# Performance work log

Measured on AMD Instinct MI355X. Metric: run time of the kernel, lower is better.

Reference implementation:

```python
import jax, jax.numpy as jnp
import numpy as np

T = 2048
C = 2048
N_HEAD = 16
HEAD_DIM = C // N_HEAD


def setup_inputs() -> dict:
    key = jax.random.key(0)
    k1, k2, k3 = jax.random.split(key, 3)
    x = jax.random.normal(k1, (T, C), dtype=jnp.float32)
    # eqx.nn.Linear weight convention: (out_features, in_features)
    W_attn = jax.random.normal(k2, (3 * C, C), dtype=jnp.float32) * (1.0 / np.sqrt(C))
    W_proj = jax.random.normal(k3, (C, C), dtype=jnp.float32) * (1.0 / np.sqrt(C))
    return {"x": x, "W_attn": W_attn, "W_proj": W_proj}


def reference(x, W_attn, W_proj):
    # qkv projection: (T, 3C)
    qkv = x @ W_attn.T
    q, k, v = jnp.split(qkv, 3, axis=-1)
    # reshape to (H, T, d)
    q = q.reshape(T, N_HEAD, HEAD_DIM).transpose(1, 0, 2)
    k = k.reshape(T, N_HEAD, HEAD_DIM).transpose(1, 0, 2)
    v = v.reshape(T, N_HEAD, HEAD_DIM).transpose(1, 0, 2)
    # scaled causal attention: (H, T, T)
    att = jnp.einsum('htd,hsd->hts', q, k)
    causal_mask = jnp.triu(jnp.ones((T, T), dtype=bool), k=1)  # mask future keys
    att = jnp.where(causal_mask, -jnp.inf, att)
    att = jax.nn.softmax(att / jnp.sqrt(jnp.float32(HEAD_DIM)), axis=-1)
    # attention output: (H, T, d) -> (T, C)
    out = jnp.einsum('hts,hsd->htd', att, v)
    out = out.transpose(1, 0, 2).reshape(T, C)
    return out @ W_proj.T
```

## Files before the change

kernel.cpp:

```cpp
#include <hip/hip_runtime.h>
#include <cstdint>

using bx8 = __attribute__((ext_vector_type(8))) __bf16;
using us8 = __attribute__((ext_vector_type(8))) unsigned short;
using us4 = __attribute__((ext_vector_type(4))) unsigned short;
using fl8 = __attribute__((ext_vector_type(8))) float;
using fx4 = __attribute__((ext_vector_type(4))) float;

static __device__ inline unsigned short f2bf(float f) {
  unsigned u = __builtin_bit_cast(unsigned, f);
  unsigned r = 0x7FFFu + ((u >> 16) & 1u);
  return (unsigned short)((u + r) >> 16);
}
static __device__ inline float bf2f(unsigned short s) {
  return __builtin_bit_cast(float, (unsigned)s << 16);
}

static __device__ inline fx4 mfma16(bx8 a, bx8 b, fx4 c) {
  return __builtin_amdgcn_mfma_f32_16x16x32_bf16(a, b, c, 0, 0, 0);
}

static __device__ inline void gload16(const void* g, void* lds) {
  __builtin_amdgcn_global_load_lds(
      (const __attribute__((address_space(1))) void*)g,
      (__attribute__((address_space(3))) void*)lds,
      16, 0, 0);
}
#define VMCNT(n) asm volatile("s_waitcnt vmcnt(" #n ")" ::: "memory")
static __device__ inline void wave_barrier() {
  __builtin_amdgcn_sched_barrier(0);
  __builtin_amdgcn_s_barrier();
  __builtin_amdgcn_sched_barrier(0);
}

#define DPP_ROR(x, k) __builtin_bit_cast(float, __builtin_amdgcn_update_dpp( \
    __builtin_bit_cast(int, x), __builtin_bit_cast(int, x), 0x120 | (k), 0xF, 0xF, false))

static __device__ inline float rowmax16(float v) {
  v = fmaxf(v, DPP_ROR(v, 1));
  v = fmaxf(v, DPP_ROR(v, 2));
  v = fmaxf(v, DPP_ROR(v, 4));
  v = fmaxf(v, DPP_ROR(v, 8));
  return v;
}
static __device__ inline float rowsum16(float v) {
  v += DPP_ROR(v, 1);
  v += DPP_ROR(v, 2);
  v += DPP_ROR(v, 4);
  v += DPP_ROR(v, 8);
  return v;
}

__global__ __launch_bounds__(256) void f2b_kernel(const float* __restrict__ in,
                                                  unsigned short* __restrict__ out,
                                                  int n) {
  int i = (blockIdx.x * 256 + threadIdx.x) * 4;
  if (i >= n) return;
  float4 v = *reinterpret_cast<const float4*>(in + i);
  ushort4 o;
  o.x = f2bf(v.x); o.y = f2bf(v.y); o.z = f2bf(v.z); o.w = f2bf(v.w);
  *reinterpret_cast<ushort4*>(out + i) = o;
}

__global__ __launch_bounds__(512, 2) void gemm256(const unsigned short* __restrict__ A,
                                                  const unsigned short* __restrict__ B,
                                                  unsigned short* __restrict__ C,
                                                  int M, int N, int K) {
  __shared__ unsigned short lds[4][2][256 * 32];

  const int tid = threadIdx.x;
  const int w = tid >> 6, l = tid & 63;
  const int l16 = l & 15, lg = l >> 4;
  const int wr = w >> 2, wc = w & 3;
  const long mb = (long)blockIdx.y * 256, nb = (long)blockIdx.x * 256;

  const int lr = l >> 2;
  const int sw = (((l & 3) ^ (lr & 3)) * 8);
  const unsigned short* Ag = A + (mb + w * 32 + lr) * (long)K + sw;
  const unsigned short* Bg = B + (nb + w * 32 + lr) * (long)K + sw;

  const int rdcol = ((lg ^ (l16 & 3)) * 16);

  const fx4 fz = {0.f, 0.f, 0.f, 0.f};
  fx4 acc[8][4];
#pragma unroll
  for (int i = 0; i < 8; ++i)
#pragma unroll
    for (int j = 0; j < 4; ++j) acc[i][j] = fz;

  const int nt = K >> 5;

  auto stage = [&](int tp) {
    const int db = tp & 3;
    const unsigned short* as = Ag + tp * 32;
    const unsigned short* bs = Bg + tp * 32;
    char* al = (char*)&lds[db][0][0] + w * 32 * 64;
    char* bl = (char*)&lds[db][1][0] + w * 32 * 64;
    gload16(as, al);
    gload16(as + 16 * (long)K, al + 1024);
    gload16(bs, bl);
    gload16(bs + 16 * (long)K, bl + 1024);
  };

  auto compute = [&](int bt) {
    const char* Ab = (const char*)&lds[bt][0][0] + (wr * 128 + l16) * 64 + rdcol;
    const char* Bb = (const char*)&lds[bt][1][0] + (wc * 64 + l16) * 64 + rdcol;
    bx8 bf[4];
#pragma unroll
    for (int nf = 0; nf < 4; ++nf)
      bf[nf] = *reinterpret_cast<const bx8*>(Bb + nf * 1024);
    __builtin_amdgcn_s_setprio(1);
#pragma unroll
    for (int mf = 0; mf < 8; ++mf) {
      bx8 av = *reinterpret_cast<const bx8*>(Ab + mf * 1024);
#pragma unroll
      for (int nf = 0; nf < 4; ++nf)
        acc[mf][nf] = mfma16(av, bf[nf], acc[mf][nf]);
    }
    __builtin_amdgcn_s_setprio(0);
  };

  stage(0); stage(1); stage(2);
  VMCNT(8);
  wave_barrier();

  int t = 0;
  for (; t < nt - 3; ++t) {
    stage(t + 3);
    compute(t & 3);
    VMCNT(8);
    wave_barrier();
  }
  compute(t & 3); VMCNT(4); wave_barrier(); ++t;
  compute(t & 3); VMCNT(0); wave_barrier(); ++t;
  compute(t & 3);

#pragma unroll
  for (int mf = 0; mf < 8; ++mf)
#pragma unroll
    for (int nf = 0; nf < 4; ++nf)
#pragma unroll
      for (int r = 0; r < 4; ++r) {
        const long row = mb + wr * 128 + mf * 16 + lg * 4 + r;
        const long col = nb + wc * 64 + nf * 16 + l16;
        C[row * N + col] = f2bf(acc[mf][nf][r]);
      }
}

template <typename T> struct RegOf { using type = us8; };
template <> struct RegOf<float>  { using type = fl8; };

template <typename T>
static __device__ inline typename RegOf<T>::type load8(const T* p) {
  return *reinterpret_cast<const typename RegOf<T>::type*>(p);
}
static __device__ inline us8 toBf(us8 v) { return v; }
static __device__ inline us8 toBf(fl8 f) {
  us8 o;
#pragma unroll
  for (int j = 0; j < 8; ++j) {
    __bf16 b = (__bf16)f[j];
    o[j] = __builtin_bit_cast(unsigned short, b);
  }
  return o;
}

template <typename TA, typename TB, bool F32OUT>
__global__ __launch_bounds__(256) void gemm_bt(const TA* __restrict__ A,
                                               const TB* __restrict__ B,
                                               void* __restrict__ Cp,
                                               int M, int N, int K) {
  __shared__ alignas(16) unsigned short As[128 * 64];
  __shared__ alignas(16) unsigned short Bs[128 * 64];
  const int tid = threadIdx.x;
  const int w = tid >> 6, l = tid & 63;
  const int l16 = l & 15, lg = l >> 4;
  const int wr = w >> 1, wc = w & 1;
  const long mb = (long)blockIdx.y * 128, nb = (long)blockIdx.x * 128;

  const fx4 fz = {0.f, 0.f, 0.f, 0.f};
  fx4 acc[4][4];
#pragma unroll
  for (int i = 0; i < 4; ++i)
#pragma unroll
    for (int j = 0; j < 4; ++j) acc[i][j] = fz;

  const int sr  = tid >> 3;
  const int sc8 = (tid & 7) * 8;
  const int wbc = sc8 * 2;

  typename RegOf<TA>::type rA[4];
  typename RegOf<TB>::type rB[4];

#pragma unroll
  for (int p = 0; p < 4; ++p) {
    const int row = p * 32 + sr;
    rA[p] = load8(A + (mb + row) * (long)K + sc8);
    rB[p] = load8(B + (nb + row) * (long)K + sc8);
  }

  for (int k0 = 0; k0 < K; k0 += 64) {
    __syncthreads();
#pragma unroll
    for (int p = 0; p < 4; ++p) {
      const int row = p * 32 + sr;
      const int eo = row * 64 + ((wbc ^ ((row & 7) << 4)) >> 1);
      *reinterpret_cast<us8*>(&As[eo]) = toBf(rA[p]);
      *reinterpret_cast<us8*>(&Bs[eo]) = toBf(rB[p]);
    }
    if (k0 + 64 < K) {
#pragma unroll
      for (int p = 0; p < 4; ++p) {
        const int row = p * 32 + sr;
        rA[p] = load8(A + (mb + row) * (long)K + k0 + 64 + sc8);
        rB[p] = load8(B + (nb + row) * (long)K + k0 + 64 + sc8);
      }
    }
    __syncthreads();
#pragma unroll
    for (int kk = 0; kk < 2; ++kk) {
      bx8 a[4], b[4];
#pragma unroll
      for (int mf = 0; mf < 4; ++mf) {
        const int ra = wr * 64 + mf * 16 + l16;
        const int bc = kk * 64 + lg * 16;
        a[mf] = *reinterpret_cast<const bx8*>(&As[ra * 64 + ((bc ^ ((ra & 7) << 4)) >> 1)]);
      }
#pragma unroll
      for (int nf = 0; nf < 4; ++nf) {
        const int rb_ = wc * 64 + nf * 16 + l16;
        const int bc = kk * 64 + lg * 16;
        b[nf] = *reinterpret_cast<const bx8*>(&Bs[rb_ * 64 + ((bc ^ ((rb_ & 7) << 4)) >> 1)]);
      }
#pragma unroll
      for (int mf = 0; mf < 4; ++mf)
#pragma unroll
        for (int nf = 0; nf < 4; ++nf)
          acc[mf][nf] = mfma16(a[mf], b[nf], acc[mf][nf]);
    }
  }

#pragma unroll
  for (int mf = 0; mf < 4; ++mf)
#pragma unroll
    for (int nf = 0; nf < 4; ++nf)
#pragma unroll
      for (int r = 0; r < 4; ++r) {
        const long row = mb + wr * 64 + mf * 16 + lg * 4 + r;
        const long col = nb + wc * 64 + nf * 16 + l16;
        if (F32OUT)
          ((float*)Cp)[row * N + col] = acc[mf][nf][r];
        else
          ((unsigned short*)Cp)[row * N + col] = f2bf(acc[mf][nf][r]);
      }
}

__global__ __launch_bounds__(256) void fa_kernel(const unsigned short* __restrict__ qkv,
                                                 unsigned short* __restrict__ Obuf,
                                                 float* __restrict__ ML) {
  __shared__ alignas(16) char smem[40960];

  const int id = blockIdx.x;
  const int h = id & 15, i = id >> 4;
  int qt, ck;
  if (i < 32)      { qt = 31 - (i >> 2); ck = i & 3; }
  else if (i < 56) { const int j = i - 32; qt = 23 - j / 3; ck = j % 3; }
  else if (i < 72) { const int j = i - 56; qt = 15 - (j >> 1); ck = j & 1; }
  else             { qt = 7 - (i - 72); ck = 0; }
  const int t0 = ck * 8;
  const int t1 = min(t0 + 8, qt + 1);
  const int qb = qt * 64;

  const int tid = threadIdx.x;
  const int w = tid >> 6, l = tid & 63;
  const int l16 = l & 15, lg = l >> 4;
  const fx4 fz = {0.f, 0.f, 0.f, 0.f};

  const int kr = tid >> 4, ksl = tid & 15;
  const int kg = tid & 15, db = tid >> 4;
  const int kc8 = ksl * 8;

  bx8 qf[4];
  {
    const long qrow = qb + w * 16 + l16;
    const unsigned short* qp = qkv + qrow * 6144L + h * 128 + lg * 8;
#pragma unroll
    for (int kc = 0; kc < 4; ++kc)
      qf[kc] = *reinterpret_cast<const bx8*>(qp + kc * 32);
  }

  fx4 o_acc[8];
#pragma unroll
  for (int i2 = 0; i2 < 8; ++i2) o_acc[i2] = fz;
  float m_r[4] = {-3e38f, -3e38f, -3e38f, -3e38f};
  float l_r[4] = {0.f, 0.f, 0.f, 0.f};

  us8 rK[4], rV[4];
  {
    const long kvb = (long)t0 * 64;
#pragma unroll
    for (int p = 0; p < 4; ++p)
      rK[p] = *reinterpret_cast<const us8*>(qkv + (kvb + p * 16 + kr) * 6144L + 2048 + h * 128 + kc8);
#pragma unroll
    for (int p = 0; p < 4; ++p)
      rV[p] = *reinterpret_cast<const us8*>(qkv + (kvb + kg * 4 + p) * 6144L + 4096 + h * 128 + db * 8);
  }

  const float sc2 = 0.1275173831f;
  char* const psb = smem + 32768 + w * 2048;

  for (int t = t0; t < t1; ++t) {
    __syncthreads();

#pragma unroll
    for (int p = 0; p < 4; ++p)
      *reinterpret_cast<us8*>(smem + (p * 16 + kr) * 256 + ((ksl ^ kr) << 4)) = rK[p];
#pragma unroll
    for (int j = 0; j < 8; ++j) {
      us4 vw = {rV[0][j], rV[1][j], rV[2][j], rV[3][j]};
      *reinterpret_cast<us4*>(smem + 16384 + (db * 8 + j) * 128 +
                              (((kg >> 1) ^ j) << 4) + ((kg & 1) << 3)) = vw;
    }

    if (t + 1 < t1) {
      const long kvb = (long)(t + 1) * 64;
#pragma unroll
      for (int p = 0; p < 4; ++p)
        rK[p] = *reinterpret_cast<const us8*>(qkv + (kvb + p * 16 + kr) * 6144L + 2048 + h * 128 + kc8);
#pragma unroll
      for (int p = 0; p < 4; ++p)
        rV[p] = *reinterpret_cast<const us8*>(qkv + (kvb + kg * 4 + p) * 6144L + 4096 + h * 128 + db * 8);
    }
    __syncthreads();

    fx4 s[4];
#pragma unroll
    for (int nf = 0; nf < 4; ++nf) s[nf] = fz;
#pragma unroll
    for (int kc = 0; kc < 4; ++kc) {
#pragma unroll
      for (int nf = 0; nf < 4; ++nf) {
        const int rl = nf * 16 + l16;
        bx8 kb = *reinterpret_cast<const bx8*>(smem + rl * 256 + (((kc * 4 + lg) ^ l16) << 4));
        s[nf] = mfma16(qf[kc], kb, s[nf]);
      }
    }

    if (t == qt) {
#pragma unroll
      for (int nf = 0; nf < 4; ++nf) {
        const int kv_abs = t * 64 + nf * 16 + l16;
#pragma unroll
        for (int r = 0; r < 4; ++r) {
          const int q_abs = qb + w * 16 + lg * 4 + r;
          if (kv_abs > q_abs) s[nf][r] = -3e38f;
        }
      }
    }

    float rm_[4];
    bool st = true;
#pragma unroll
    for (int r = 0; r < 4; ++r) {
      float rm = fmaxf(fmaxf(s[0][r], s[1][r]), fmaxf(s[2][r], s[3][r]));
      rm_[r] = rowmax16(rm);
      st = st && (rm_[r] - m_r[r] <= 62.7f);
    }
    float pv[4][4];
    if (__all(st ? 1 : 0)) {
#pragma unroll
      for (int r = 0; r < 4; ++r) {
        float rs = 0.f;
#pragma unroll
        for (int nf = 0; nf < 4; ++nf) {
          const float p = exp2f((s[nf][r] - m_r[r]) * sc2);
          pv[nf][r] = p;
          rs += p;
        }
        l_r[r] += rowsum16(rs);
      }
    } else {
#pragma unroll
      for (int r = 0; r < 4; ++r) {
        const float mn = fmaxf(m_r[r], rm_[r]);
        const float fac = exp2f((m_r[r] - mn) * sc2);
        m_r[r] = mn;
        float rs = 0.f;
#pragma unroll
        for (int nf = 0; nf < 4; ++nf) {
          const float p = exp2f((s[nf][r] - mn) * sc2);
          pv[nf][r] = p;
          rs += p;
        }
        l_r[r] = l_r[r] * fac + rowsum16(rs);
#pragma unroll
        for (int nf = 0; nf < 8; ++nf) o_acc[nf][r] *= fac;
      }
    }

#pragma unroll
    for (int nf = 0; nf < 4; ++nf)
#pragma unroll
      for (int r = 0; r < 4; ++r) {
        const int ro = lg * 4 + r;
        *reinterpret_cast<unsigned short*>(
            psb + ro * 128 + (((nf * 2 + (l16 >> 3)) ^ (ro & 7)) << 4) + ((l16 & 7) << 1)) =
            __builtin_bit_cast(unsigned short, (__bf16)pv[nf][r]);
      }

    bx8 pa[2];
#pragma unroll
    for (int kc = 0; kc < 2; ++kc)
      pa[kc] = *reinterpret_cast<const bx8*>(psb + l16 * 128 + (((kc * 4 + lg) ^ (l16 & 7)) << 4));

#pragma unroll
    for (int nf = 0; nf < 8; ++nf) {
#pragma unroll
      for (int kc = 0; kc < 2; ++kc) {
        bx8 vb = *reinterpret_cast<const bx8*>(smem + 16384 + (nf * 16 + l16) * 128 +
                                               (((kc * 4 + lg) ^ (l16 & 7)) << 4));
        o_acc[nf] = mfma16(pa[kc], vb, o_acc[nf]);
      }
    }
  }

  unsigned short* ob = Obuf + (long)id * 8192;
#pragma unroll
  for (int nf = 0; nf < 8; ++nf)
#pragma unroll
    for (int r = 0; r < 4; ++r) {
      const int row = w * 16 + lg * 4 + r;
      ob[row * 128 + nf * 16 + l16] = f2bf(o_acc[nf][r]);
    }
  if (l16 == 0) {
#pragma unroll
    for (int r = 0; r < 4; ++r) {
      const int row = w * 16 + lg * 4 + r;
      ML[((long)id * 64 + row) * 2 + 0] = m_r[r];
      ML[((long)id * 64 + row) * 2 + 1] = l_r[r];
    }
  }
}

__global__ __launch_bounds__(256) void fa_combine(const unsigned short* __restrict__ Obuf,
                                                  const float* __restrict__ ML,
                                                  unsigned short* __restrict__ out) {
  const int p = blockIdx.x;
  const int qt = p >> 4, h = p & 15;
  const int nc = (qt + 8) >> 3;
  const int tid = threadIdx.x;
  const int row = tid >> 2;
  const int c0 = (tid & 3) * 32;
  const float sc2 = 0.1275173831f;

  int ids[4];
#pragma unroll
  for (int k = 0; k < 4; ++k) {
    int ib;
    if (qt >= 24)      ib = (31 - qt) * 4 + k;
    else if (qt >= 16) ib = 32 + (23 - qt) * 3 + k;
    else if (qt >= 8)  ib = 56 + (15 - qt) * 2 + k;
    else               ib = 72 + (7 - qt);
    ids[k] = ib * 16 + h;
  }

  float mk[4], lk[4];
  float m = -3e38f;
#pragma unroll
  for (int k = 0; k < 4; ++k)
    if (k < nc) {
      mk[k] = ML[((long)ids[k] * 64 + row) * 2 + 0];
      lk[k] = ML[((long)ids[k] * 64 + row) * 2 + 1];
      m = fmaxf(m, mk[k]);
    }
  float fk[4], denom = 0.f;
#pragma unroll
  for (int k = 0; k < 4; ++k)
    if (k < nc) {
      fk[k] = exp2f((mk[k] - m) * sc2);
      denom += lk[k] * fk[k];
    }
  const float inv = 1.0f / denom;

  float acc[32];
#pragma unroll
  for (int j = 0; j < 32; ++j) acc[j] = 0.f;
#pragma unroll
  for (int k = 0; k < 4; ++k)
    if (k < nc) {
      const unsigned short* ob = Obuf + (long)ids[k] * 8192 + row * 128 + c0;
      const float f = fk[k];
#pragma unroll
      for (int jj = 0; jj < 4; ++jj) {
        us8 a = *reinterpret_cast<const us8*>(ob + jj * 8);
#pragma unroll
        for (int j2 = 0; j2 < 8; ++j2) acc[jj * 8 + j2] += bf2f(a[j2]) * f;
      }
    }

  unsigned short* dst = out + (long)(qt * 64 + row) * 2048 + h * 128 + c0;
#pragma unroll
  for (int jj = 0; jj < 4; ++jj) {
    ushort4 o0, o1;
    o0.x = f2bf(acc[jj * 8 + 0] * inv);
    o0.y = f2bf(acc[jj * 8 + 1] * inv);
    o0.z = f2bf(acc[jj * 8 + 2] * inv);
    o0.w = f2bf(acc[jj * 8 + 3] * inv);
    o1.x = f2bf(acc[jj * 8 + 4] * inv);
    o1.y = f2bf(acc[jj * 8 + 5] * inv);
    o1.z = f2bf(acc[jj * 8 + 6] * inv);
    o1.w = f2bf(acc[jj * 8 + 7] * inv);
    *reinterpret_cast<ushort4*>(dst + jj * 8) = o0;
    *reinterpret_cast<ushort4*>(dst + jj * 8 + 4) = o1;
  }
}

extern "C" void kernel_launch(void* const* d_in, const int* in_sizes, int n_in,
                              void* d_out, int out_size, void* d_ws, size_t ws_size,
                              hipStream_t stream) {
  const float* x  = (const float*)d_in[0];
  const float* Wa = (const float*)d_in[1];
  const float* Wp = (const float*)d_in[2];
  float* out = (float*)d_out;
  char* ws = (char*)d_ws;

  unsigned short* wab   = (unsigned short*)(ws);
  unsigned short* qkvb  = (unsigned short*)(ws + (24ull << 20));
  unsigned short* xb    = (unsigned short*)(ws + (48ull << 20));
  unsigned short* Obuf  = (unsigned short*)(ws);
  float*          ML    = (float*)(ws + (20ull << 20));
  unsigned short* attnb = (unsigned short*)(ws + (48ull << 20));

  f2b_kernel<<<4096, 256, 0, stream>>>(x, xb, 2048 * 2048);
  f2b_kernel<<<12288, 256, 0, stream>>>(Wa, wab, 6144 * 2048);

  gemm256<<<dim3(24, 8), 512, 0, stream>>>(xb, wab, qkvb, 2048, 6144, 2048);

  fa_kernel<<<1280, 256, 0, stream>>>(qkvb, Obuf, ML);

  fa_combine<<<512, 256, 0, stream>>>(Obuf, ML, attnb);

  gemm_bt<unsigned short, float, true><<<dim3(16, 16), 256, 0, stream>>>(attnb, Wp, (void*)out, 2048, 2048, 2048);
}
```

Before: 180.7 us.

## Double flash-attention query tile to 128 rows per block for K/V reuse

Each attention block now processes 128 query rows instead of 64, with every wave handling two 16-row query fragments that share the same K and V fragments loaded from LDS. The split-K scheduling table, Obuf/ML layout and combine kernel indexing are rewritten for the new tile size, and the grid is halved. This halves K/V global and LDS traffic per query row and amortizes the synchronisation, at the cost of double the accumulator registers (lower occupancy), wasted work on the diagonal tile pairs, and fewer blocks to fill the GPU.

After: 204.0 us. 1.13x slower.

```diff
diff --git a/kernel.cpp b/kernel.cpp
--- a/kernel.cpp
+++ b/kernel.cpp
@@ -258,18 +258,19 @@
 __global__ __launch_bounds__(256) void fa_kernel(const unsigned short* __restrict__ qkv,
                                                  unsigned short* __restrict__ Obuf,
                                                  float* __restrict__ ML) {
-  __shared__ alignas(16) char smem[40960];
+  __shared__ alignas(16) char smem[49152];
 
   const int id = blockIdx.x;
   const int h = id & 15, i = id >> 4;
-  int qt, ck;
-  if (i < 32)      { qt = 31 - (i >> 2); ck = i & 3; }
-  else if (i < 56) { const int j = i - 32; qt = 23 - j / 3; ck = j % 3; }
-  else if (i < 72) { const int j = i - 56; qt = 15 - (j >> 1); ck = j & 1; }
-  else             { qt = 7 - (i - 72); ck = 0; }
+  int tau, ck;
+  if (i < 16)      { tau = 15 - (i >> 2); ck = i & 3; }
+  else if (i < 28) { const int j = i - 16; tau = 11 - j / 3; ck = j % 3; }
+  else if (i < 36) { const int j = i - 28; tau = 7 - (j >> 1); ck = j & 1; }
+  else             { tau = 3 - (i - 36); ck = 0; }
+  const int ntk = 2 * tau + 2;
   const int t0 = ck * 8;
-  const int t1 = min(t0 + 8, qt + 1);
-  const int qb = qt * 64;
+  const int t1 = min(t0 + 8, ntk);
+  const int qb = tau * 128;
 
   const int tid = threadIdx.x;
   const int w = tid >> 6, l = tid & 63;
@@ -280,20 +281,26 @@
   const int kg = tid & 15, db = tid >> 4;
   const int kc8 = ksl * 8;
 
-  bx8 qf[4];
-  {
-    const long qrow = qb + w * 16 + l16;
+  bx8 qf[2][4];
+#pragma unroll
+  for (int qh = 0; qh < 2; ++qh) {
+    const long qrow = qb + w * 32 + qh * 16 + l16;
     const unsigned short* qp = qkv + qrow * 6144L + h * 128 + lg * 8;
 #pragma unroll
     for (int kc = 0; kc < 4; ++kc)
-      qf[kc] = *reinterpret_cast<const bx8*>(qp + kc * 32);
-  }
-
-  fx4 o_acc[8];
-#pragma unroll
-  for (int i2 = 0; i2 < 8; ++i2) o_acc[i2] = fz;
-  float m_r[4] = {-3e38f, -3e38f, -3e38f, -3e38f};
-  float l_r[4] = {0.f, 0.f, 0.f, 0.f};
+      qf[qh][kc] = *reinterpret_cast<const bx8*>(qp + kc * 32);
+  }
+
+  fx4 o_acc[2][8];
+#pragma unroll
+  for (int qh = 0; qh < 2; ++qh)
+#pragma unroll
+    for (int i2 = 0; i2 < 8; ++i2) o_acc[qh][i2] = fz;
+  float m_r[2][4], l_r[2][4];
+#pragma unroll
+  for (int qh = 0; qh < 2; ++qh)
+#pragma unroll
+    for (int r = 0; r < 4; ++r) { m_r[qh][r] = -3e38f; l_r[qh][r] = 0.f; }
 
   us8 rK[4], rV[4];
   {
@@ -307,7 +314,7 @@
   }
 
   const float sc2 = 0.1275173831f;
-  char* const psb = smem + 32768 + w * 2048;
+  char* const psb = smem + 32768 + w * 4096;
 
   for (int t = t0; t < t1; ++t) {
     __syncthreads();
@@ -333,85 +340,101 @@
     }
     __syncthreads();
 
-    fx4 s[4];
-#pragma unroll
-    for (int nf = 0; nf < 4; ++nf) s[nf] = fz;
+    fx4 s[2][4];
+#pragma unroll
+    for (int qh = 0; qh < 2; ++qh)
+#pragma unroll
+      for (int nf = 0; nf < 4; ++nf) s[qh][nf] = fz;
 #pragma unroll
     for (int kc = 0; kc < 4; ++kc) {
 #pragma unroll
       for (int nf = 0; nf < 4; ++nf) {
         const int rl = nf * 16 + l16;
         bx8 kb = *reinterpret_cast<const bx8*>(smem + rl * 256 + (((kc * 4 + lg) ^ l16) << 4));
-        s[nf] = mfma16(qf[kc], kb, s[nf]);
-      }
-    }
-
-    if (t == qt) {
-#pragma unroll
-      for (int nf = 0; nf < 4; ++nf) {
-        const int kv_abs = t * 64 + nf * 16 + l16;
+        s[0][nf] = mfma16(qf[0][kc], kb, s[0][nf]);
+        s[1][nf] = mfma16(qf[1][kc], kb, s[1][nf]);
+      }
+    }
+
+    if (t >= ntk - 2) {
+#pragma unroll
+      for (int qh = 0; qh < 2; ++qh)
+#pragma unroll
+        for (int nf = 0; nf < 4; ++nf) {
+          const int kv_abs = t * 64 + nf * 16 + l16;
+#pragma unroll
+          for (int r = 0; r < 4; ++r) {
+            const int q_abs = qb + w * 32 + qh * 16 + lg * 4 + r;
+            if (kv_abs > q_abs) s[qh][nf][r] = -3e38f;
+          }
+        }
+    }
+
+    float rm_[2][4];
+    bool st = true;
+#pragma unroll
+    for (int qh = 0; qh < 2; ++qh)
+#pragma unroll
+      for (int r = 0; r < 4; ++r) {
+        float rm = fmaxf(fmaxf(s[qh][0][r], s[qh][1][r]), fmaxf(s[qh][2][r], s[qh][3][r]));
+        rm_[qh][r] = rowmax16(rm);
+        st = st && (rm_[qh][r] - m_r[qh][r] <= 62.7f);
+      }
+    float pv[2][4][4];
+    if (__all(st ? 1 : 0)) {
+#pragma unroll
+      for (int qh = 0; qh < 2; ++qh)
 #pragma unroll
         for (int r = 0; r < 4; ++r) {
-          const int q_abs = qb + w * 16 + lg * 4 + r;
-          if (kv_abs > q_abs) s[nf][r] = -3e38f;
+          float rs = 0.f;
+#pragma unroll
+          for (int nf = 0; nf < 4; ++nf) {
+            const float p = exp2f((s[qh][nf][r] - m_r[qh][r]) * sc2);
+            pv[qh][nf][r] = p;
+            rs += p;
+          }
+          l_r[qh][r] += rowsum16(rs);
         }
-      }
-    }
-
-    float rm_[4];
-    bool st = true;
-#pragma unroll
-    for (int r = 0; r < 4; ++r) {
-      float rm = fmaxf(fmaxf(s[0][r], s[1][r]), fmaxf(s[2][r], s[3][r]));
-      rm_[r] = rowmax16(rm);
-      st = st && (rm_[r] - m_r[r] <= 62.7f);
-    }
-    float pv[4][4];
-    if (__all(st ? 1 : 0)) {
-#pragma unroll
-      for (int r = 0; r < 4; ++r) {
-        float rs = 0.f;
-#pragma unroll
-        for (int nf = 0; nf < 4; ++nf) {
-          const float p = exp2f((s[nf][r] - m_r[r]) * sc2);
-          pv[nf][r] = p;
-          rs += p;
+    } else {
+#pragma unroll
+      for (int qh = 0; qh < 2; ++qh)
+#pragma unroll
+        for (int r = 0; r < 4; ++r) {
+          const float mn = fmaxf(m_r[qh][r], rm_[qh][r]);
+          const float fac = exp2f((m_r[qh][r] - mn) * sc2);
+          m_r[qh][r] = mn;
+          float rs = 0.f;
+#pragma unroll
+          for (int nf = 0; nf < 4; ++nf) {
+            const float p = exp2f((s[qh][nf][r] - mn) * sc2);
+            pv[qh][nf][r] = p;
+            rs += p;
+          }
+          l_r[qh][r] = l_r[qh][r] * fac + rowsum16(rs);
+#pragma unroll
+          for (int nf = 0; nf < 8; ++nf) o_acc[qh][nf][r] *= fac;
         }
-        l_r[r] += rowsum16(rs);
-      }
-    } else {
-#pragma unroll
-      for (int r = 0; r < 4; ++r) {
-        const float mn = fmaxf(m_r[r], rm_[r]);
-        const float fac = exp2f((m_r[r] - mn) * sc2);
-        m_r[r] = mn;
-        float rs = 0.f;
-#pragma unroll
-        for (int nf = 0; nf < 4; ++nf) {
-          const float p = exp2f((s[nf][r] - mn) * sc2);
-          pv[nf][r] = p;
-          rs += p;
+    }
+
+#pragma unroll
+    for (int qh = 0; qh < 2; ++qh)
+#pragma unroll
+      for (int nf = 0; nf < 4; ++nf)
+#pragma unroll
+        for (int r = 0; r < 4; ++r) {
+          const int ro = qh * 16 + lg * 4 + r;
+          *reinterpret_cast<unsigned short*>(
+              psb + ro * 128 + (((nf * 2 + (l16 >> 3)) ^ (ro & 7)) << 4) + ((l16 & 7) << 1)) =
+              __builtin_bit_cast(unsigned short, (__bf16)pv[qh][nf][r]);
         }
-        l_r[r] = l_r[r] * fac + rowsum16(rs);
-#pragma unroll
-        for (int nf = 0; nf < 8; ++nf) o_acc[nf][r] *= fac;
-      }
-    }
-
-#pragma unroll
-    for (int nf = 0; nf < 4; ++nf)
-#pragma unroll
-      for (int r = 0; r < 4; ++r) {
-        const int ro = lg * 4 + r;
-        *reinterpret_cast<unsigned short*>(
-            psb + ro * 128 + (((nf * 2 + (l16 >> 3)) ^ (ro & 7)) << 4) + ((l16 & 7) << 1)) =
-            __builtin_bit_cast(unsigned short, (__bf16)pv[nf][r]);
-      }
-
-    bx8 pa[2];
-#pragma unroll
-    for (int kc = 0; kc < 2; ++kc)
-      pa[kc] = *reinterpret_cast<const bx8*>(psb + l16 * 128 + (((kc * 4 + lg) ^ (l16 & 7)) << 4));
+
+    bx8 pa[2][2];
+#pragma unroll
+    for (int qh = 0; qh < 2; ++qh)
+#pragma unroll
+      for (int kc = 0; kc < 2; ++kc)
+        pa[qh][kc] = *reinterpret_cast<const bx8*>(
+            psb + (qh * 16 + l16) * 128 + (((kc * 4 + lg) ^ (l16 & 7)) << 4));
 
 #pragma unroll
     for (int nf = 0; nf < 8; ++nf) {
@@ -419,26 +442,31 @@
       for (int kc = 0; kc < 2; ++kc) {
         bx8 vb = *reinterpret_cast<const bx8*>(smem + 16384 + (nf * 16 + l16) * 128 +
                                                (((kc * 4 + lg) ^ (l16 & 7)) << 4));
-        o_acc[nf] = mfma16(pa[kc], vb, o_acc[nf]);
-      }
-    }
-  }
-
-  unsigned short* ob = Obuf + (long)id * 8192;
-#pragma unroll
-  for (int nf = 0; nf < 8; ++nf)
-#pragma unroll
-    for (int r = 0; r < 4; ++r) {
-      const int row = w * 16 + lg * 4 + r;
-      ob[row * 128 + nf * 16 + l16] = f2bf(o_acc[nf][r]);
-    }
+        o_acc[0][nf] = mfma16(pa[0][kc], vb, o_acc[0][nf]);
+        o_acc[1][nf] = mfma16(pa[1][kc], vb, o_acc[1][nf]);
+      }
+    }
+  }
+
+  unsigned short* ob = Obuf + (long)id * 16384;
+#pragma unroll
+  for (int qh = 0; qh < 2; ++qh)
+#pragma unroll
+    for (int nf = 0; nf < 8; ++nf)
+#pragma unroll
+      for (int r = 0; r < 4; ++r) {
+        const int row = w * 32 + qh * 16 + lg * 4 + r;
+        ob[row * 128 + nf * 16 + l16] = f2bf(o_acc[qh][nf][r]);
+      }
   if (l16 == 0) {
 #pragma unroll
-    for (int r = 0; r < 4; ++r) {
-      const int row = w * 16 + lg * 4 + r;
-      ML[((long)id * 64 + row) * 2 + 0] = m_r[r];
-      ML[((long)id * 64 + row) * 2 + 1] = l_r[r];
-    }
+    for (int qh = 0; qh < 2; ++qh)
+#pragma unroll
+      for (int r = 0; r < 4; ++r) {
+        const int row = w * 32 + qh * 16 + lg * 4 + r;
+        ML[((long)id * 128 + row) * 2 + 0] = m_r[qh][r];
+        ML[((long)id * 128 + row) * 2 + 1] = l_r[qh][r];
+      }
   }
 }
 
@@ -446,10 +474,11 @@
                                                   const float* __restrict__ ML,
                                                   unsigned short* __restrict__ out) {
   const int p = blockIdx.x;
-  const int qt = p >> 4, h = p & 15;
-  const int nc = (qt + 8) >> 3;
+  const int th = p >> 1, half = p & 1;
+  const int tau = th >> 4, h = th & 15;
+  const int nc = (tau >= 12) ? 4 : (tau >= 8) ? 3 : (tau >= 4) ? 2 : 1;
   const int tid = threadIdx.x;
-  const int row = tid >> 2;
+  const int row = half * 64 + (tid >> 2);
   const int c0 = (tid & 3) * 32;
   const float sc2 = 0.1275173831f;
 
@@ -457,10 +486,10 @@
 #pragma unroll
   for (int k = 0; k < 4; ++k) {
     int ib;
-    if (qt >= 24)      ib = (31 - qt) * 4 + k;
-    else if (qt >= 16) ib = 32 + (23 - qt) * 3 + k;
-    else if (qt >= 8)  ib = 56 + (15 - qt) * 2 + k;
-    else               ib = 72 + (7 - qt);
+    if (tau >= 12)     ib = (15 - tau) * 4 + k;
+    else if (tau >= 8) ib = 16 + (11 - tau) * 3 + k;
+    else if (tau >= 4) ib = 28 + (7 - tau) * 2 + k;
+    else               ib = 36 + (3 - tau);
     ids[k] = ib * 16 + h;
   }
 
@@ -469,8 +498,8 @@
 #pragma unroll
   for (int k = 0; k < 4; ++k)
     if (k < nc) {
-      mk[k] = ML[((long)ids[k] * 64 + row) * 2 + 0];
-      lk[k] = ML[((long)ids[k] * 64 + row) * 2 + 1];
+      mk[k] = ML[((long)ids[k] * 128 + row) * 2 + 0];
+      lk[k] = ML[((long)ids[k] * 128 + row) * 2 + 1];
       m = fmaxf(m, mk[k]);
     }
   float fk[4], denom = 0.f;
@@ -488,7 +517,7 @@
 #pragma unroll
   for (int k = 0; k < 4; ++k)
     if (k < nc) {
-      const unsigned short* ob = Obuf + (long)ids[k] * 8192 + row * 128 + c0;
+      const unsigned short* ob = Obuf + (long)ids[k] * 16384 + row * 128 + c0;
       const float f = fk[k];
 #pragma unroll
       for (int jj = 0; jj < 4; ++jj) {
@@ -498,7 +527,7 @@
       }
     }
 
-  unsigned short* dst = out + (long)(qt * 64 + row) * 2048 + h * 128 + c0;
+  unsigned short* dst = out + (long)(tau * 128 + row) * 2048 + h * 128 + c0;
 #pragma unroll
   for (int jj = 0; jj < 4; ++jj) {
     ushort4 o0, o1;
@@ -536,7 +565,7 @@
 
   gemm256<<<dim3(24, 8), 512, 0, stream>>>(xb, wab, qkvb, 2048, 6144, 2048);
 
-  fa_kernel<<<1280, 256, 0, stream>>>(qkvb, Obuf, ML);
+  fa_kernel<<<640, 256, 0, stream>>>(qkvb, Obuf, ML);
 
   fa_combine<<<512, 256, 0, stream>>>(Obuf, ML, attnb);
 
```
